# Kernel optimization log

Hardware: AMD Instinct MI355X
Metric: run time of the kernel (lower is better)

The kernel has to match this reference:

```python
import jax, jax.numpy as jnp
import numpy as np

B, TG, A, N_RULES, K = 32, 131072, 8, 64, 16384


def setup_inputs() -> dict:
    key = jax.random.key(0)
    k1, k2, k3, k4 = jax.random.split(key, 4)
    body = jax.random.normal(k1, (B, TG, A), dtype=jnp.float32)
    mask = (jax.random.uniform(k2, (B, TG)) < 0.9).astype(jnp.float32)
    rule_idx = jax.random.randint(k3, (B, TG), 0, N_RULES, dtype=jnp.int64)
    # pre-drawn uniform noise standing in for torch.rand in training mode
    rand = jax.random.uniform(k4, (B, TG), dtype=jnp.float32)
    return {"body": body, "mask": mask, "rule_idx": rule_idx, "rand": rand, "k": K}


def reference(body, mask, rule_idx, rand, k):
    # training path: scores = U[0,1) * mask  (invalid groundings get score 0)
    scores = rand * mask                      # [B, TG]
    _, idx = jax.lax.top_k(scores, k)         # [B, k] indices into TG
    body_sel = jnp.take_along_axis(body, idx[..., None], axis=1)  # [B, k, A]
    mask_sel = jnp.take_along_axis(mask, idx, axis=1)             # [B, k]
    rule_sel = jnp.take_along_axis(rule_idx, idx, axis=1)         # [B, k]
    return body_sel, mask_sel, rule_sel
```

## Files before the change

### kernel.cpp

```cpp
#include <hip/hip_runtime.h>
#include <stdint.h>


namespace {
constexpr int kB    = 32;
constexpr int kTG   = 131072;
constexpr int kA    = 8;
constexpr int kK    = 16384;
constexpr int kBins = 1024;
constexpr int kTiles = 16;
constexpr int kTileElems = kTG / kTiles;
constexpr int kStageCap = 3072;
constexpr int kRowCap   = kTiles * kStageCap;
constexpr uint32_t kBase = 0xC0800000u;
constexpr uint32_t kSpan = (uint32_t)kBins << 12;
}

__device__ __forceinline__ uint32_t score_key(float s) {
    return ~__float_as_uint(s);
}

__global__ __launch_bounds__(256) void histstage_kernel(
        const float* __restrict__ rnd, const float* __restrict__ msk,
        uint32_t* __restrict__ hist, uint64_t* __restrict__ stage,
        uint32_t* __restrict__ stagecnt) {
    __shared__ uint32_t h[kBins];
    __shared__ uint32_t scount;
    int blk = blockIdx.x;
    int r = blk >> 4, t = blk & 15;
    int tid = threadIdx.x, lane = tid & 63;
    for (int i = tid; i < kBins; i += 256) h[i] = 0;
    if (tid == 0) scount = 0;
    __syncthreads();
    size_t base = (size_t)r * kTG + (size_t)t * kTileElems;
    const float4* r4 = (const float4*)(rnd + base);
    const float4* m4 = (const float4*)(msk + base);
    uint64_t* sblk = stage + (size_t)blk * kStageCap;
    #pragma unroll
    for (int s = 0; s < 8; ++s) {
        int fi = s * 256 + tid;
        float4 a = r4[fi], b = m4[fi];
        uint32_t key[4];
        key[0] = score_key(a.x * b.x); key[1] = score_key(a.y * b.y);
        key[2] = score_key(a.z * b.z); key[3] = score_key(a.w * b.w);
        uint32_t eidx = (uint32_t)(t * kTileElems + fi * 4);
        #pragma unroll
        for (int j = 0; j < 4; ++j) {
            uint32_t rel = key[j] - kBase;
            bool sel = rel < kSpan;
            uint64_t bal = __ballot((int)sel);
            if (bal) {
                int leader = __ffsll((unsigned long long)bal) - 1;
                uint32_t wbase = 0;
                if (lane == leader)
                    wbase = atomicAdd(&scount, (uint32_t)__popcll(bal));
                wbase = (uint32_t)__shfl((int)wbase, leader);
                if (sel) {
                    uint32_t pos = wbase +
                        (uint32_t)__popcll(bal & ((1ull << lane) - 1ull));
                    if (pos < (uint32_t)kStageCap) {
                        sblk[pos] = ((uint64_t)key[j] << 32) | (eidx + j);
                        atomicAdd(&h[rel >> 12], 1u);
                    }
                }
            }
        }
    }
    __syncthreads();
    uint32_t* out = hist + (size_t)blk * kBins;
    for (int i = tid; i < kBins; i += 256) out[i] = h[i];
    if (tid == 0) {
        uint32_t n = scount;
        stagecnt[blk] = n > (uint32_t)kStageCap ? (uint32_t)kStageCap : n;
    }
}

__global__ __launch_bounds__(256) void scan_kernel(
        const uint32_t* __restrict__ hist, uint32_t* __restrict__ offs,
        uint32_t* __restrict__ rowbase, uint32_t* __restrict__ ncand) {
    __shared__ uint32_t tsum[256];
    int r = blockIdx.x, tid = threadIdx.x;
    uint32_t v[4], c[4];
    uint32_t s = 0;
    #pragma unroll
    for (int j = 0; j < 4; ++j) {
        uint32_t b = tid * 4 + j, x = 0;
        for (int t = 0; t < kTiles; ++t)
            x += hist[((size_t)r * kTiles + t) * kBins + b];
        c[j] = x; s += x; v[j] = s;
    }
    tsum[tid] = s;
    __syncthreads();
    for (int off = 1; off < 256; off <<= 1) {
        uint32_t u = (tid >= off) ? tsum[tid - off] : 0u;
        __syncthreads();
        tsum[tid] += u;
        __syncthreads();
    }
    uint32_t excl = tsum[tid] - s;
    #pragma unroll
    for (int j = 0; j < 4; ++j) {
        uint32_t b = tid * 4 + j;
        uint32_t bb = excl + v[j] - c[j];
        rowbase[r * kBins + b] = bb;
        uint32_t run = bb;
        for (int t = 0; t < kTiles; ++t) {
            size_t p = ((size_t)r * kTiles + t) * kBins + b;
            offs[p] = run;
            run += hist[p];
        }
    }
    if (tid == 255) ncand[r] = tsum[255];
}

__global__ __launch_bounds__(256) void scatter_kernel(
        const uint64_t* __restrict__ stage, const uint32_t* __restrict__ stagecnt,
        const uint32_t* __restrict__ offs, uint64_t* __restrict__ cand) {
    __shared__ uint32_t run[kBins];
    int blk = blockIdx.x;
    int r = blk >> 4;
    int tid = threadIdx.x;
    for (int i = tid; i < kBins; i += 256)
        run[i] = offs[(size_t)blk * kBins + i];
    __syncthreads();
    uint32_t n = stagecnt[blk];
    const uint64_t* sblk = stage + (size_t)blk * kStageCap;
    uint64_t* crow = cand + (size_t)r * kRowCap;
    for (uint32_t i = tid; i < n; i += 256) {
        uint64_t rec = sblk[i];
        uint32_t d = ((uint32_t)(rec >> 32) - kBase) >> 12;
        uint32_t pos = atomicAdd(&run[d], 1u);
        crow[pos] = rec;
    }
}

__device__ __forceinline__ uint64_t cswap(uint64_t v, int j, bool dir, int lane) {
    uint64_t pv = (uint64_t)__shfl_xor((long long)v, j);
    uint64_t mn = v < pv ? v : pv;
    uint64_t mx = v < pv ? pv : v;
    return (((lane & j) == 0) == dir) ? mn : mx;
}

__global__ __launch_bounds__(256) void sortgather_kernel(
        const uint32_t* __restrict__ rowbase, const uint32_t* __restrict__ ncand,
        const uint64_t* __restrict__ cand, const float* __restrict__ body,
        const int* __restrict__ rule, int rule_is_i64,
        float* __restrict__ out) {
    int g = blockIdx.x * 4 + (threadIdx.x >> 6);
    int lane = threadIdx.x & 63;
    int r = g >> 10, b = g & (kBins - 1);
    uint32_t start = rowbase[r * kBins + b];
    if (start >= (uint32_t)kK) return;
    uint32_t end = (b + 1 < kBins) ? rowbase[r * kBins + b + 1] : ncand[r];
    uint32_t n = end - start;
    if (n == 0) return;
    if (n > 128u) n = 128u;
    const uint64_t* seg = cand + (size_t)r * kRowCap + start;
    uint64_t v0 = ~0ull, v1 = ~0ull;
    if (lane < (int)n) v0 = seg[lane];
    if (n > 64u && lane + 64 < (int)n) v1 = seg[lane + 64];
    if (n <= 64u) {
        for (int k = 2; k <= 64; k <<= 1) {
            bool dir = ((lane & k) == 0);
            for (int j = k >> 1; j > 0; j >>= 1) v0 = cswap(v0, j, dir, lane);
        }
    } else {
        for (int k = 2; k <= 64; k <<= 1) {
            bool d0 = ((lane & k) == 0);
            bool d1 = (((lane + 64) & k) == 0);
            for (int j = k >> 1; j > 0; j >>= 1) {
                v0 = cswap(v0, j, d0, lane);
                v1 = cswap(v1, j, d1, lane);
            }
        }
        uint64_t mn = v0 < v1 ? v0 : v1, mx = v0 < v1 ? v1 : v0;
        v0 = mn; v1 = mx;
        for (int j = 32; j > 0; j >>= 1) {
            v0 = cswap(v0, j, true, lane);
            v1 = cswap(v1, j, true, lane);
        }
    }
    size_t mask_off = (size_t)kB * kK * kA;
    size_t rule_off = mask_off + (size_t)kB * kK;
    #pragma unroll
    for (int h = 0; h < 2; ++h) {
        int i = lane + h * 64;
        uint64_t v = h ? v1 : v0;
        if (i < (int)n) {
            uint32_t jrank = start + (uint32_t)i;
            if (jrank < (uint32_t)kK) {
                uint32_t idx = (uint32_t)v;
                size_t src = (size_t)r * kTG + idx;
                const float4* bp = (const float4*)(body + src * kA);
                float4 b0 = bp[0], b1 = bp[1];
                size_t og = (size_t)r * kK + jrank;
                float4* op = (float4*)(out + og * kA);
                op[0] = b0; op[1] = b1;
                out[mask_off + og] = 1.0f;
                int rv = rule_is_i64 ? rule[src * 2] : rule[src];
                out[rule_off + og] = (float)rv;
            }
        }
    }
}

extern "C" void kernel_launch(void* const* d_in, const int* in_sizes, int n_in,
                              void* d_out, int out_size, void* d_ws, size_t ws_size,
                              hipStream_t stream) {
    const float* body = (const float*)d_in[0];
    const float* msk  = (const float*)d_in[1];
    const int*   rule = (const int*)d_in[2];
    const float* rnd  = (const float*)d_in[3];
    int rule_is_i64 = (in_sizes[2] == 2 * in_sizes[1]) ? 1 : 0;

    uint32_t* hist     = (uint32_t*)d_ws;
    uint32_t* offs     = hist + (size_t)kB * kTiles * kBins;
    uint32_t* rowbase  = offs + (size_t)kB * kTiles * kBins;
    uint32_t* ncand    = rowbase + (size_t)kB * kBins;
    uint32_t* stagecnt = ncand + kB;
    size_t hdr_u32 = 2 * (size_t)kB * kTiles * kBins
                   + (size_t)kB * kBins + kB + kB * kTiles;
    hdr_u32 = (hdr_u32 + 1) & ~(size_t)1;
    uint64_t* stage = (uint64_t*)((uint32_t*)d_ws + hdr_u32);
    uint64_t* cand  = stage + (size_t)kB * kTiles * kStageCap;

    histstage_kernel<<<kB * kTiles, 256, 0, stream>>>(rnd, msk, hist, stage, stagecnt);
    scan_kernel<<<kB, 256, 0, stream>>>(hist, offs, rowbase, ncand);
    scatter_kernel<<<kB * kTiles, 256, 0, stream>>>(stage, stagecnt, offs, cand);
    sortgather_kernel<<<(kB * kBins) / 4, 256, 0, stream>>>(
        rowbase, ncand, cand, body, rule, rule_is_i64, (float*)d_out);
}
```

Before: 59.05 us.

## Fuse scan into scatter and pack candidate records into 32-bit keys

Merges the per-row scan and the scatter into one kernel launched per tile. Each block recomputes the row's bin prefix sums and its own tile offset straight from the histograms, which removes the offs buffer and one kernel launch. Candidate records are packed into 32 bits (12 low key bits within the bin plus a 17-bit index), which halves candidate traffic and lets the bitonic sort shuffle 32-bit values. In exchange the scan work is done redundantly 16 times per row, and the packed form depends on TG fitting in 17 bits and on 4096 key values per bin.

Result: faster. 55.32 us (-6.3%).

```diff
diff --git a/kernel.cpp b/kernel.cpp
--- a/kernel.cpp
+++ b/kernel.cpp
@@ -75,19 +75,26 @@
     }
 }
 
-__global__ __launch_bounds__(256) void scan_kernel(
-        const uint32_t* __restrict__ hist, uint32_t* __restrict__ offs,
+__global__ __launch_bounds__(256) void scanscatter_kernel(
+        const uint32_t* __restrict__ hist, const uint64_t* __restrict__ stage,
+        const uint32_t* __restrict__ stagecnt, uint32_t* __restrict__ cand,
         uint32_t* __restrict__ rowbase, uint32_t* __restrict__ ncand) {
+    __shared__ uint32_t run[kBins];
     __shared__ uint32_t tsum[256];
-    int r = blockIdx.x, tid = threadIdx.x;
-    uint32_t v[4], c[4];
+    int blk = blockIdx.x;
+    int r = blk >> 4, t = blk & 15;
+    int tid = threadIdx.x;
+    uint32_t v[4], c[4], pre[4];
     uint32_t s = 0;
     #pragma unroll
     for (int j = 0; j < 4; ++j) {
-        uint32_t b = tid * 4 + j, x = 0;
-        for (int t = 0; t < kTiles; ++t)
-            x += hist[((size_t)r * kTiles + t) * kBins + b];
-        c[j] = x; s += x; v[j] = s;
+        uint32_t b = tid * 4 + j, x = 0, xt = 0;
+        for (int tt = 0; tt < kTiles; ++tt) {
+            uint32_t hh = hist[((size_t)r * kTiles + tt) * kBins + b];
+            x += hh;
+            if (tt < t) xt += hh;
+        }
+        c[j] = x; s += x; v[j] = s; pre[j] = xt;
     }
     tsum[tid] = s;
     __syncthreads();
@@ -101,49 +108,34 @@
     #pragma unroll
     for (int j = 0; j < 4; ++j) {
         uint32_t b = tid * 4 + j;
-        uint32_t bb = excl + v[j] - c[j];
-        rowbase[r * kBins + b] = bb;
-        uint32_t run = bb;
-        for (int t = 0; t < kTiles; ++t) {
-            size_t p = ((size_t)r * kTiles + t) * kBins + b;
-            offs[p] = run;
-            run += hist[p];
-        }
-    }
-    if (tid == 255) ncand[r] = tsum[255];
-}
-
-__global__ __launch_bounds__(256) void scatter_kernel(
-        const uint64_t* __restrict__ stage, const uint32_t* __restrict__ stagecnt,
-        const uint32_t* __restrict__ offs, uint64_t* __restrict__ cand) {
-    __shared__ uint32_t run[kBins];
-    int blk = blockIdx.x;
-    int r = blk >> 4;
-    int tid = threadIdx.x;
-    for (int i = tid; i < kBins; i += 256)
-        run[i] = offs[(size_t)blk * kBins + i];
+        uint32_t rb = excl + v[j] - c[j];
+        run[b] = rb + pre[j];
+        if (t == 0) rowbase[r * kBins + b] = rb;
+    }
+    if (t == 0 && tid == 255) ncand[r] = tsum[255];
     __syncthreads();
     uint32_t n = stagecnt[blk];
     const uint64_t* sblk = stage + (size_t)blk * kStageCap;
-    uint64_t* crow = cand + (size_t)r * kRowCap;
+    uint32_t* crow = cand + (size_t)r * kRowCap;
     for (uint32_t i = tid; i < n; i += 256) {
         uint64_t rec = sblk[i];
-        uint32_t d = ((uint32_t)(rec >> 32) - kBase) >> 12;
+        uint32_t rel = (uint32_t)(rec >> 32) - kBase;
+        uint32_t d = rel >> 12;
         uint32_t pos = atomicAdd(&run[d], 1u);
-        crow[pos] = rec;
-    }
-}
-
-__device__ __forceinline__ uint64_t cswap(uint64_t v, int j, bool dir, int lane) {
-    uint64_t pv = (uint64_t)__shfl_xor((long long)v, j);
-    uint64_t mn = v < pv ? v : pv;
-    uint64_t mx = v < pv ? pv : v;
+        crow[pos] = ((rel & 0xFFFu) << 17) | ((uint32_t)rec & 0x1FFFFu);
+    }
+}
+
+__device__ __forceinline__ uint32_t cswap32(uint32_t v, int j, bool dir, int lane) {
+    uint32_t pv = (uint32_t)__shfl_xor((int)v, j);
+    uint32_t mn = v < pv ? v : pv;
+    uint32_t mx = v < pv ? pv : v;
     return (((lane & j) == 0) == dir) ? mn : mx;
 }
 
 __global__ __launch_bounds__(256) void sortgather_kernel(
         const uint32_t* __restrict__ rowbase, const uint32_t* __restrict__ ncand,
-        const uint64_t* __restrict__ cand, const float* __restrict__ body,
+        const uint32_t* __restrict__ cand, const float* __restrict__ body,
         const int* __restrict__ rule, int rule_is_i64,
         float* __restrict__ out) {
     int g = blockIdx.x * 4 + (threadIdx.x >> 6);
@@ -155,29 +147,29 @@
     uint32_t n = end - start;
     if (n == 0) return;
     if (n > 128u) n = 128u;
-    const uint64_t* seg = cand + (size_t)r * kRowCap + start;
-    uint64_t v0 = ~0ull, v1 = ~0ull;
+    const uint32_t* seg = cand + (size_t)r * kRowCap + start;
+    uint32_t v0 = 0xFFFFFFFFu, v1 = 0xFFFFFFFFu;
     if (lane < (int)n) v0 = seg[lane];
     if (n > 64u && lane + 64 < (int)n) v1 = seg[lane + 64];
     if (n <= 64u) {
         for (int k = 2; k <= 64; k <<= 1) {
             bool dir = ((lane & k) == 0);
-            for (int j = k >> 1; j > 0; j >>= 1) v0 = cswap(v0, j, dir, lane);
+            for (int j = k >> 1; j > 0; j >>= 1) v0 = cswap32(v0, j, dir, lane);
         }
     } else {
         for (int k = 2; k <= 64; k <<= 1) {
             bool d0 = ((lane & k) == 0);
             bool d1 = (((lane + 64) & k) == 0);
             for (int j = k >> 1; j > 0; j >>= 1) {
-                v0 = cswap(v0, j, d0, lane);
-                v1 = cswap(v1, j, d1, lane);
+                v0 = cswap32(v0, j, d0, lane);
+                v1 = cswap32(v1, j, d1, lane);
             }
         }
-        uint64_t mn = v0 < v1 ? v0 : v1, mx = v0 < v1 ? v1 : v0;
+        uint32_t mn = v0 < v1 ? v0 : v1, mx = v0 < v1 ? v1 : v0;
         v0 = mn; v1 = mx;
         for (int j = 32; j > 0; j >>= 1) {
-            v0 = cswap(v0, j, true, lane);
-            v1 = cswap(v1, j, true, lane);
+            v0 = cswap32(v0, j, true, lane);
+            v1 = cswap32(v1, j, true, lane);
         }
     }
     size_t mask_off = (size_t)kB * kK * kA;
@@ -185,11 +177,11 @@
     #pragma unroll
     for (int h = 0; h < 2; ++h) {
         int i = lane + h * 64;
-        uint64_t v = h ? v1 : v0;
+        uint32_t v = h ? v1 : v0;
         if (i < (int)n) {
             uint32_t jrank = start + (uint32_t)i;
             if (jrank < (uint32_t)kK) {
-                uint32_t idx = (uint32_t)v;
+                uint32_t idx = v & 0x1FFFFu;
                 size_t src = (size_t)r * kTG + idx;
                 const float4* bp = (const float4*)(body + src * kA);
                 float4 b0 = bp[0], b1 = bp[1];
@@ -214,19 +206,19 @@
     int rule_is_i64 = (in_sizes[2] == 2 * in_sizes[1]) ? 1 : 0;
 
     uint32_t* hist     = (uint32_t*)d_ws;
-    uint32_t* offs     = hist + (size_t)kB * kTiles * kBins;
-    uint32_t* rowbase  = offs + (size_t)kB * kTiles * kBins;
+    uint32_t* rowbase  = hist + (size_t)kB * kTiles * kBins;
     uint32_t* ncand    = rowbase + (size_t)kB * kBins;
     uint32_t* stagecnt = ncand + kB;
-    size_t hdr_u32 = 2 * (size_t)kB * kTiles * kBins
-                   + (size_t)kB * kBins + kB + kB * kTiles;
+    uint32_t* cand     = stagecnt + kB * kTiles;
+    size_t hdr_u32 = (size_t)kB * kTiles * kBins + (size_t)kB * kBins
+                   + kB + kB * kTiles + (size_t)kB * kRowCap;
     hdr_u32 = (hdr_u32 + 1) & ~(size_t)1;
     uint64_t* stage = (uint64_t*)((uint32_t*)d_ws + hdr_u32);
-    uint64_t* cand  = stage + (size_t)kB * kTiles * kStageCap;
-
-    histstage_kernel<<<kB * kTiles, 256, 0, stream>>>(rnd, msk, hist, stage, stagecnt);
-    scan_kernel<<<kB, 256, 0, stream>>>(hist, offs, rowbase, ncand);
-    scatter_kernel<<<kB * kTiles, 256, 0, stream>>>(stage, stagecnt, offs, cand);
+
+    histstage_kernel<<<kB * kTiles, 256, 0, stream>>>(
+        rnd, msk, hist, stage, stagecnt);
+    scanscatter_kernel<<<kB * kTiles, 256, 0, stream>>>(
+        hist, stage, stagecnt, cand, rowbase, ncand);
     sortgather_kernel<<<(kB * kBins) / 4, 256, 0, stream>>>(
         rowbase, ncand, cand, body, rule, rule_is_i64, (float*)d_out);
 }
```
